# Kernel optimization log

Measured on AMD Instinct MI355X. Metric: run time of the kernel, lower is better.

The kernel has to match this reference:

```python
import jax, jax.numpy as jnp
import numpy as np

THRESH = 0.5
DECAY = 0.2
D_IN = 784
H1 = 2048
H2 = 10
K = 10
U = D_IN + H1
L = 128
B = 1024


def setup_inputs() -> dict:
    key = jax.random.key(0)
    ks = jax.random.split(key, 6)
    inp = jax.random.uniform(ks[0], (B, D_IN), dtype=jnp.float32)
    W1 = jax.random.normal(ks[1], (H1, D_IN), dtype=jnp.float32) * 0.05
    b1 = jnp.zeros((H1,), dtype=jnp.float32)
    W2 = jax.random.normal(ks[2], (H2, H1), dtype=jnp.float32) * 0.05
    b2 = jnp.zeros((H2,), dtype=jnp.float32)
    # core_mem_all[k][u][0] -> sparse-ish per-unit vector, [1] -> count
    core_mem_vec = (jax.random.uniform(ks[3], (K, U, L)) > 0.7).astype(jnp.float32)
    core_mem_cnt = jax.random.randint(ks[4], (K, U), 0, 5).astype(jnp.int32)
    return {"input": inp, "W1": W1, "b1": b1, "W2": W2, "b2": b2,
            "core_mem_vec": core_mem_vec, "core_mem_cnt": core_mem_cnt,
            "time_window": 20}


def act_fun(mem):
    # spike = Heaviside(mem - thresh)
    return (mem > THRESH).astype(mem.dtype)


def reference(input, W1, b1, W2, b2, core_mem_vec, core_mem_cnt, time_window):
    batch, d_in = input.shape
    h1 = W1.shape[0]
    h2 = W2.shape[0]
    Lv = core_mem_vec.shape[-1]

    # Precompute, per (core k, unit u): contribution to count_add_1 / count_add_2
    # when unit u spikes. count_add_1 += (last nonzero index of temp) - 1 when cnt>0;
    # count_add_2 += cnt when cnt>0. Sum over cores up front (loop order irrelevant).
    nz = core_mem_vec != 0                                     # [K,U,L]
    has = nz.any(-1)
    last_idx = Lv - 1 - jnp.argmax(nz[..., ::-1].astype(jnp.int32), axis=-1)  # [K,U]
    active = (core_mem_cnt > 0) & has
    val1 = jnp.where(active, last_idx - 1, 0).sum(0).astype(jnp.float32)      # [U]
    val2 = jnp.where(core_mem_cnt > 0, core_mem_cnt, 0).sum(0).astype(jnp.float32)
    v1x, v1h = val1[:d_in], val1[d_in:]
    v2x, v2h = val2[:d_in], val2[d_in:]

    key = jax.random.key(42)

    def step(carry, t):
        h1m, h1s, h2m, h2s, h2sum, a1, a2, cs = carry
        # Bernoulli rate encoding of the input image
        x = (input > jax.random.uniform(jax.random.fold_in(key, t), input.shape)).astype(jnp.float32)
        # mem_update: mem = mem*decay*(1-spike) + W x + b ; spike = mem > thresh
        h1m = h1m * DECAY * (1.0 - h1s) + x @ W1.T + b1
        h1s = act_fun(h1m)
        h2m = h2m * DECAY * (1.0 - h2s) + h1s @ W2.T + b2
        h2s = act_fun(h2m)
        h2sum = h2sum + h2s
        # vectorized core-memory gather/count: sum per-unit precomputed values
        # over all spiking units, across the batch
        xs = x.sum(0)      # [784] spike counts per input unit this step
        hs = h1s.sum(0)    # [h1]
        a1 = a1 + xs @ v1x + hs @ v1h
        a2 = a2 + xs @ v2x + hs @ v2h
        cs = cs + xs.sum() + hs.sum()
        return (h1m, h1s, h2m, h2s, h2sum, a1, a2, cs), None

    z1 = jnp.zeros((batch, h1), dtype=jnp.float32)
    z2 = jnp.zeros((batch, h2), dtype=jnp.float32)
    carry = (z1, z1, z2, z2, z2, jnp.float32(0), jnp.float32(0), jnp.float32(0))
    carry, _ = jax.lax.scan(step, carry, jnp.arange(time_window))
    _, _, _, _, h2sum, a1, a2, cs = carry
    outputs = h2sum / time_window
    return outputs, a1, a2, cs
```

## Files before the change

kernel.cpp:

```cpp
#include <hip/hip_runtime.h>
#include <cstdint>
#include <cstddef>

static constexpr int D_IN = 784;
static constexpr int H1   = 2048;
static constexpr int H2   = 10;
static constexpr int KK   = 10;
static constexpr int UU   = 2832;
static constexpr int LL   = 128;
static constexpr int BB   = 1024;
static constexpr int TT   = 20;
static constexpr int HALF = BB * D_IN / 2;
static constexpr int KS   = 13;
static constexpr int NLIMB = 3;
static constexpr int NT16 = 128;
static constexpr int MT16 = 64;
static constexpr int PANEL16 = KS * NLIMB * 64;
static constexpr int XA_MT = KS * 64;
static constexpr int NPART_GEN = 2080;
static constexpr int NPART_H1  = 512;
static constexpr int NPART = NPART_GEN + NPART_H1;

static constexpr int BLK_VALS  = UU / 4;
static constexpr int BLK_W2T   = H1 / 256;
static constexpr int BLK_LIMBS = (NT16 * KS) / 4;
static constexpr int BLK_TRANS = 16 * 13;
static constexpr int SETUP_BLOCKS = BLK_VALS + BLK_W2T + BLK_LIMBS + BLK_TRANS;

typedef int v4i  __attribute__((ext_vector_type(4)));

#define MFMA16 __builtin_amdgcn_mfma_i32_16x16x64_i8

__device__ __forceinline__ uint32_t rotl32(uint32_t x, int d) {
  return (x << d) | (x >> (32 - d));
}
__device__ __forceinline__ void threefry2x32(uint32_t k0, uint32_t k1,
                                             uint32_t& x0, uint32_t& x1) {
  uint32_t ks2 = k0 ^ k1 ^ 0x1BD11BDAu;
  x0 += k0; x1 += k1;
#define TF_R(r) { x0 += x1; x1 = rotl32(x1, (r)); x1 ^= x0; }
  TF_R(13) TF_R(15) TF_R(26) TF_R(6)
  x0 += k1;  x1 += ks2 + 1u;
  TF_R(17) TF_R(29) TF_R(16) TF_R(24)
  x0 += ks2; x1 += k0 + 2u;
  TF_R(13) TF_R(15) TF_R(26) TF_R(6)
  x0 += k0;  x1 += k1 + 3u;
  TF_R(17) TF_R(29) TF_R(16) TF_R(24)
  x0 += k1;  x1 += ks2 + 4u;
  TF_R(13) TF_R(15) TF_R(26) TF_R(6)
  x0 += ks2; x1 += k0 + 5u;
#undef TF_R
}
__device__ __forceinline__ float bits_to_unif(uint32_t b) {
  uint32_t fb = (b >> 9) | 0x3F800000u;
  return __uint_as_float(fb) - 1.0f;
}

__device__ __forceinline__ double wave_red(double v) {
  #pragma unroll
  for (int off = 32; off > 0; off >>= 1) v += __shfl_down(v, off, 64);
  return v;
}
__device__ __forceinline__ void block_store3(double s0, double s1, double s2,
                                             double* slot) {
  __shared__ double lds[3][8];
  int lane = threadIdx.x & 63, w = threadIdx.x >> 6;
  int nw = (int)(blockDim.x >> 6);
  s0 = wave_red(s0); s1 = wave_red(s1); s2 = wave_red(s2);
  if (lane == 0) { lds[0][w] = s0; lds[1][w] = s1; lds[2][w] = s2; }
  __syncthreads();
  if (threadIdx.x == 0) {
    double t0 = 0, t1 = 0, t2 = 0;
    for (int i = 0; i < nw; i++) { t0 += lds[0][i]; t1 += lds[1][i]; t2 += lds[2][i]; }
    slot[0] = t0; slot[1] = t1; slot[2] = t2;
  }
}

__global__ __launch_bounds__(256)
void setup(const float* __restrict__ cmv, const int* __restrict__ cmc,
           float* __restrict__ v1, float* __restrict__ v2,
           const float* __restrict__ W2, float* __restrict__ W2T,
           const float* __restrict__ W1, v4i* __restrict__ W1L,
           const float* __restrict__ input, float2* __restrict__ inT2) {
  int bx = blockIdx.x;
  if (bx < BLK_VALS) {
    int u = bx * 4 + (threadIdx.x >> 6);
    int lane = threadIdx.x & 63;
    float acc1 = 0.0f, acc2 = 0.0f;
    for (int k = 0; k < KK; k++) {
      const float* p = cmv + ((size_t)k * UU + u) * LL;
      float a = p[lane];
      float b = p[lane + 64];
      unsigned long long mlo = __ballot(a != 0.0f);
      unsigned long long mhi = __ballot(b != 0.0f);
      int c = cmc[k * UU + u];
      if (c > 0) {
        int last = mhi ? (127 - __builtin_clzll(mhi))
                       : (mlo ? (63 - __builtin_clzll(mlo)) : -1);
        if (last >= 0) acc1 += (float)(last - 1);
        acc2 += (float)c;
      }
    }
    if (lane == 0) { v1[u] = acc1; v2[u] = acc2; }
  } else if (bx < BLK_VALS + BLK_W2T) {
    int i = (bx - BLK_VALS) * 256 + threadIdx.x;
    #pragma unroll
    for (int j = 0; j < H2; j++) W2T[i * H2 + j] = W2[j * H1 + i];
  } else if (bx < BLK_VALS + BLK_W2T + BLK_LIMBS) {
    int tid = (bx - BLK_VALS - BLK_W2T) * 256 + threadIdx.x;
    int lane = tid & 63;
    int tw = tid >> 6;
    int nt = tw / KS, s = tw - nt * KS;
    int n = (nt << 4) + (lane & 15);
    int k0 = (s << 6) + ((lane >> 4) << 4);
    bool valid = (k0 < D_IN);
    union { v4i v; signed char b[16]; } d[NLIMB];
    #pragma unroll
    for (int j = 0; j < 16; j++) {
      long long F = 0;
      if (valid) {
        double w = (double)W1[(size_t)n * D_IN + k0 + j];
        F = llround(w * 0x1p24);
        if (F >  8355711LL) F =  8355711LL;
        if (F < -8421504LL) F = -8421504LL;
      }
      #pragma unroll
      for (int l = 0; l < NLIMB; l++) {
        int dig = (int)((F + 128) & 255) - 128;
        d[l].b[j] = (signed char)dig;
        F = (F - dig) >> 8;
      }
    }
    #pragma unroll
    for (int l = 0; l < NLIMB; l++)
      W1L[(size_t)((nt * KS + s) * NLIMB + l) * 64 + lane] = d[l].v;
  } else {
    int tile = bx - (BLK_VALS + BLK_W2T + BLK_LIMBS);
    int tm = tile / 13, tk = tile % 13;
    int mb = tm * 32, k0 = tk * 64;
    int ncol = (tk == 12) ? 16 : 64;
    __shared__ float ts[64][65];
    int tid = threadIdx.x;
    int nc4 = (tk == 12) ? 4 : 16;
    for (int idx = tid; idx < 64 * nc4; idx += 256) {
      int r = idx / nc4, c4 = idx % nc4;
      int m = mb + (r & 31) + ((r >> 5) << 9);
      const float4* src = (const float4*)(input + (size_t)m * D_IN + k0 + c4 * 4);
      float4 vq = *src;
      ts[r][c4 * 4 + 0] = vq.x; ts[r][c4 * 4 + 1] = vq.y;
      ts[r][c4 * 4 + 2] = vq.z; ts[r][c4 * 4 + 3] = vq.w;
    }
    __syncthreads();
    for (int idx = tid; idx < ncol * 32; idx += 256) {
      int kr = idx >> 5, mc = idx & 31;
      inT2[(size_t)(k0 + kr) * 512 + mb + mc] =
          make_float2(ts[mc][kr], ts[32 + mc][kr]);
    }
  }
}

__global__ __launch_bounds__(256)
void gen_all(const float2* __restrict__ inT2, v4i* __restrict__ XA,
             const float* __restrict__ v1, const float* __restrict__ v2,
             double* __restrict__ gpart) {
  int gw = blockIdx.x * 4 + (threadIdx.x >> 6);
  int lane = threadIdx.x & 63;
  int t = gw / (32 * KS);
  int rem = gw - t * (32 * KS);
  int mt = rem / KS, s = rem - mt * KS;
  int m = (mt << 4) + (lane & 15);
  int k0 = (s << 6) + ((lane >> 4) << 4);
  uint32_t f0 = 0u, f1 = (uint32_t)t;
  threefry2x32(0u, 42u, f0, f1);
  union { v4i v; unsigned char b[16]; } r0, r1;
  double s0 = 0, s1 = 0, s2 = 0;
  if (k0 < D_IN) {
    #pragma unroll
    for (int j = 0; j < 16; j++) {
      int k = k0 + j;
      uint32_t c0 = (uint32_t)(m * D_IN + k), c1 = c0 + (uint32_t)HALF;
      threefry2x32(f0, f1, c0, c1);
      float u0 = bits_to_unif(c0), u1 = bits_to_unif(c1);
      float2 iv = inT2[(size_t)k * 512 + m];
      unsigned char x0 = (iv.x > u0) ? 1 : 0;
      unsigned char x1 = (iv.y > u1) ? 1 : 0;
      r0.b[j] = x0; r1.b[j] = x1;
      double xsum = (double)(x0 + x1);
      s0 += xsum * (double)v1[k];
      s1 += xsum * (double)v2[k];
      s2 += xsum;
    }
  } else {
    r0.v = (v4i){0, 0, 0, 0};
    r1.v = (v4i){0, 0, 0, 0};
  }
  XA[(size_t)((t * MT16 + mt) * KS + s) * 64 + lane] = r0.v;
  XA[(size_t)((t * MT16 + mt + 32) * KS + s) * 64 + lane] = r1.v;
  block_store3(s0, s1, s2, gpart + 3 * (size_t)blockIdx.x);
}

__global__ __launch_bounds__(512, 4)
void h1_all(const v4i* __restrict__ XA, const v4i* __restrict__ W1L,
            const float* __restrict__ b1, uint16_t* __restrict__ bits16,
            const float* __restrict__ v1, const float* __restrict__ v2,
            double* __restrict__ gpart) {
  extern __shared__ v4i bl[];
  int lane = threadIdx.x & 63, wv = threadIdx.x >> 6;
  int id = blockIdx.x + (blockIdx.y << 6);
  int xcd = id & 7;
  int ntb = ((id >> 3) << 1) | (xcd >> 2);
  int mg = xcd & 3;
  int mt0 = (mg << 4) + (wv << 1);
  {
    const v4i* wp = W1L + (size_t)ntb * PANEL16;
    for (int i = threadIdx.x; i < PANEL16; i += 512) bl[i] = wp[i];
  }
  __syncthreads();

  int col = lane & 15;
  int gn = (ntb << 4) + col;
  float bias = b1[gn];
  double v1n = (double)v1[D_IN + gn], v2n = (double)v2[D_IN + gn];
  int scnt = 0;
  float m00 = 0, m01 = 0, m02 = 0, m03 = 0;
  float m10 = 0, m11 = 0, m12 = 0, m13 = 0;
  const v4i* bq = bl + lane;
  int rowg = (lane >> 4) << 2;

  #pragma unroll 1
  for (int t = 0; t < TT; t++) {
    const v4i* a0 = XA + (size_t)((t * MT16 + mt0) * KS) * 64 + lane;
    const v4i* a1 = a0 + KS * 64;
    v4i c00 = {}, c01 = {}, c02 = {};
    v4i c10 = {}, c11 = {}, c12 = {};
    __builtin_amdgcn_s_setprio(1);
    #pragma unroll
    for (int s = 0; s < KS; s++) {
      v4i A0 = a0[s * 64], A1 = a1[s * 64];
      v4i B0 = bq[(s * NLIMB + 0) * 64];
      v4i B1 = bq[(s * NLIMB + 1) * 64];
      v4i B2 = bq[(s * NLIMB + 2) * 64];
      c00 = MFMA16(A0, B0, c00, 0, 0, 0);
      c10 = MFMA16(A1, B0, c10, 0, 0, 0);
      c01 = MFMA16(A0, B1, c01, 0, 0, 0);
      c11 = MFMA16(A1, B1, c11, 0, 0, 0);
      c02 = MFMA16(A0, B2, c02, 0, 0, 0);
      c12 = MFMA16(A1, B2, c12, 0, 0, 0);
    }
    __builtin_amdgcn_s_setprio(0);
    #pragma unroll
    for (int tile = 0; tile < 2; tile++) {
      const v4i& q0 = tile ? c10 : c00;
      const v4i& q1 = tile ? c11 : c01;
      const v4i& q2 = tile ? c12 : c02;
      int gmb = ((mt0 + tile) << 4);
      uint16_t* bp = bits16 + ((size_t)t * BB + gmb) * NT16 + ntb;
      #pragma unroll
      for (int r = 0; r < 4; r++) {
        int val = (int)((uint32_t)q0[r] + ((uint32_t)q1[r] << 8)
                        + ((uint32_t)q2[r] << 16));
        float dot = (float)val * 0x1p-24f + bias;
        float mp = tile ? (r == 0 ? m10 : r == 1 ? m11 : r == 2 ? m12 : m13)
                        : (r == 0 ? m00 : r == 1 ? m01 : r == 2 ? m02 : m03);
        float mnew = (mp > 0.5f) ? dot : fmaf(mp, 0.2f, dot);
        bool sp = (mnew > 0.5f);
        if (tile) { if (r == 0) m10 = mnew; else if (r == 1) m11 = mnew;
                    else if (r == 2) m12 = mnew; else m13 = mnew; }
        else      { if (r == 0) m00 = mnew; else if (r == 1) m01 = mnew;
                    else if (r == 2) m02 = mnew; else m03 = mnew; }
        unsigned long long bm = __ballot(sp);
        if ((lane & 15) == 0)
          bp[(size_t)(rowg + r) * NT16] = (uint16_t)(bm >> lane);
        scnt += sp ? 1 : 0;
      }
    }
  }
  double sc = (double)scnt;
  block_store3(sc * v1n, sc * v2n, sc, gpart + 3 * (size_t)(NPART_GEN + id));
}

__global__ __launch_bounds__(256)
void h2_all(const uint32_t* __restrict__ bits, const float* __restrict__ W2T,
            const float* __restrict__ b2, const double* __restrict__ gpart,
            float* __restrict__ out) {
  int lane = threadIdx.x & 63, wq = threadIdx.x >> 6;
  int b0 = blockIdx.x * 2;
  float w[8][10];
  #pragma unroll
  for (int c = 0; c < 8; c++) {
    int n = (wq << 9) + (c << 6) + lane;
    #pragma unroll
    for (int j = 0; j < 10; j++) w[c][j] = W2T[(size_t)n * H2 + j];
  }
  float m = 0.0f, sp = 0.0f, sm = 0.0f;
  float b2v = (lane < 10) ? b2[lane] : 0.0f;
  __shared__ float part[4][2][10];
  #pragma unroll 1
  for (int t = 0; t < TT; t++) {
    const uint32_t* bt = bits + (size_t)t * (BB * 64);
    #pragma unroll
    for (int r = 0; r < 2; r++) {
      uint32_t myw = bt[(size_t)(b0 + r) * 64 + (wq << 4) + (lane & 15)];
      float p[10];
      #pragma unroll
      for (int j = 0; j < 10; j++) p[j] = 0.0f;
      #pragma unroll
      for (int c = 0; c < 8; c++) {
        uint32_t wd = __shfl(myw, (c << 1) + (lane >> 5), 64);
        float f = (float)((wd >> (lane & 31)) & 1u);
        #pragma unroll
        for (int j = 0; j < 10; j++) p[j] += f * w[c][j];
      }
      #pragma unroll
      for (int j = 0; j < 10; j++) {
        float v = p[j];
        #pragma unroll
        for (int off = 32; off > 0; off >>= 1) v += __shfl_xor(v, off, 64);
        p[j] = v;
      }
      if (lane == 0) {
        #pragma unroll
        for (int j = 0; j < 10; j++) part[wq][r][j] = p[j];
      }
    }
    __syncthreads();
    if (wq < 2 && lane < 10) {
      float red = part[0][wq][lane] + part[1][wq][lane]
                + part[2][wq][lane] + part[3][wq][lane];
      m = m * 0.2f * (1.0f - sp) + red + b2v;
      sp = (m > 0.5f) ? 1.0f : 0.0f;
      sm += sp;
    }
    __syncthreads();
  }
  if (wq < 2 && lane < 10)
    out[(size_t)(b0 + wq) * H2 + lane] = (float)((double)sm / (double)TT);

  if (blockIdx.x == 0) {
    double t0 = 0, t1 = 0, t2 = 0;
    for (int i = threadIdx.x; i < NPART; i += 256) {
      t0 += gpart[3 * (size_t)i];
      t1 += gpart[3 * (size_t)i + 1];
      t2 += gpart[3 * (size_t)i + 2];
    }
    __shared__ double fin[3][4];
    t0 = wave_red(t0); t1 = wave_red(t1); t2 = wave_red(t2);
    if (lane == 0) { fin[0][wq] = t0; fin[1][wq] = t1; fin[2][wq] = t2; }
    __syncthreads();
    if (threadIdx.x == 0) {
      double a = 0, b = 0, cc = 0;
      #pragma unroll
      for (int i = 0; i < 4; i++) { a += fin[0][i]; b += fin[1][i]; cc += fin[2][i]; }
      out[(size_t)BB * H2 + 0] = (float)a;
      out[(size_t)BB * H2 + 1] = (float)b;
      out[(size_t)BB * H2 + 2] = (float)cc;
    }
  }
}

extern "C" void kernel_launch(void* const* d_in, const int* in_sizes, int n_in,
                              void* d_out, int out_size, void* d_ws, size_t ws_size,
                              hipStream_t stream) {
  (void)in_sizes; (void)n_in; (void)out_size; (void)ws_size;
  const float* input = (const float*)d_in[0];
  const float* W1    = (const float*)d_in[1];
  const float* b1    = (const float*)d_in[2];
  const float* W2    = (const float*)d_in[3];
  const float* b2    = (const float*)d_in[4];
  const float* cmv   = (const float*)d_in[5];
  const int*   cmc   = (const int*)d_in[6];

  char* base = (char*)d_ws;
  float*  v1   = (float*)(base + 0);
  float*  v2   = (float*)(base + 11328);
  float*  W2T  = (float*)(base + 22656);
  v4i*    W1L  = (v4i*)(base + 104576);
  v4i*    XA   = (v4i*)(base + 5216384);
  char*   bitsb = base + 22255744;
  double* gpart = (double*)(base + 27498624);
  float2* inT2 = (float2*)bitsb;
  uint16_t* bits16 = (uint16_t*)bitsb;
  uint32_t* bits32 = (uint32_t*)bitsb;

  setup<<<SETUP_BLOCKS, 256, 0, stream>>>(cmv, cmc, v1, v2, W2, W2T, W1, W1L,
                                          input, inT2);
  gen_all<<<NPART_GEN, 256, 0, stream>>>(inT2, XA, v1, v2, gpart);
  h1_all<<<dim3(64, 8), 512, PANEL16 * 16, stream>>>(XA, W1L, b1, bits16, v1, v2,
                                                     gpart);
  h2_all<<<BB / 2, 256, 0, stream>>>(bits32, W2T, b2, gpart, (float*)d_out);
}
```

Baseline: 283.8 us.

## Fuse spike generation into setup kernel and defer input-count reduction to h1

Spike generation is folded into the setup kernel, which removes one kernel launch and the transposed input buffer. Inputs are now read directly as float4 rows. Per-input-unit spike counts are accumulated with ballot/popc and LDS atomics into a per-block count array, and h1_all reduces these counts and applies v1/v2 in its epilogue. This drops the per-block double reductions from the generation stage, but adds extra reads and a sync to h1_all and leaves the input loads uncoalesced along rows.

```diff
diff --git a/kernel.cpp b/kernel.cpp
--- a/kernel.cpp
+++ b/kernel.cpp
@@ -16,16 +16,13 @@
 static constexpr int NT16 = 128;
 static constexpr int MT16 = 64;
 static constexpr int PANEL16 = KS * NLIMB * 64;
-static constexpr int XA_MT = KS * 64;
-static constexpr int NPART_GEN = 2080;
-static constexpr int NPART_H1  = 512;
-static constexpr int NPART = NPART_GEN + NPART_H1;
+static constexpr int NPART = 512;
+static constexpr int NGENB = 2080;
 
 static constexpr int BLK_VALS  = UU / 4;
 static constexpr int BLK_W2T   = H1 / 256;
 static constexpr int BLK_LIMBS = (NT16 * KS) / 4;
-static constexpr int BLK_TRANS = 16 * 13;
-static constexpr int SETUP_BLOCKS = BLK_VALS + BLK_W2T + BLK_LIMBS + BLK_TRANS;
+static constexpr int PREP_BLOCKS = BLK_VALS + BLK_W2T + BLK_LIMBS + NGENB;
 
 typedef int v4i  __attribute__((ext_vector_type(4)));
 
@@ -77,11 +74,12 @@
 }
 
 __global__ __launch_bounds__(256)
-void setup(const float* __restrict__ cmv, const int* __restrict__ cmc,
-           float* __restrict__ v1, float* __restrict__ v2,
-           const float* __restrict__ W2, float* __restrict__ W2T,
-           const float* __restrict__ W1, v4i* __restrict__ W1L,
-           const float* __restrict__ input, float2* __restrict__ inT2) {
+void prep(const float* __restrict__ cmv, const int* __restrict__ cmc,
+          float* __restrict__ v1, float* __restrict__ v2,
+          const float* __restrict__ W2, float* __restrict__ W2T,
+          const float* __restrict__ W1, v4i* __restrict__ W1L,
+          const float* __restrict__ input, v4i* __restrict__ XA,
+          int* __restrict__ xcp) {
   int bx = blockIdx.x;
   if (bx < BLK_VALS) {
     int u = bx * 4 + (threadIdx.x >> 6);
@@ -135,75 +133,62 @@
     for (int l = 0; l < NLIMB; l++)
       W1L[(size_t)((nt * KS + s) * NLIMB + l) * 64 + lane] = d[l].v;
   } else {
-    int tile = bx - (BLK_VALS + BLK_W2T + BLK_LIMBS);
-    int tm = tile / 13, tk = tile % 13;
-    int mb = tm * 32, k0 = tk * 64;
-    int ncol = (tk == 12) ? 16 : 64;
-    __shared__ float ts[64][65];
-    int tid = threadIdx.x;
-    int nc4 = (tk == 12) ? 4 : 16;
-    for (int idx = tid; idx < 64 * nc4; idx += 256) {
-      int r = idx / nc4, c4 = idx % nc4;
-      int m = mb + (r & 31) + ((r >> 5) << 9);
-      const float4* src = (const float4*)(input + (size_t)m * D_IN + k0 + c4 * 4);
-      float4 vq = *src;
-      ts[r][c4 * 4 + 0] = vq.x; ts[r][c4 * 4 + 1] = vq.y;
-      ts[r][c4 * 4 + 2] = vq.z; ts[r][c4 * 4 + 3] = vq.w;
-    }
-    __syncthreads();
-    for (int idx = tid; idx < ncol * 32; idx += 256) {
-      int kr = idx >> 5, mc = idx & 31;
-      inT2[(size_t)(k0 + kr) * 512 + mb + mc] =
-          make_float2(ts[mc][kr], ts[32 + mc][kr]);
-    }
-  }
-}
-
-__global__ __launch_bounds__(256)
-void gen_all(const float2* __restrict__ inT2, v4i* __restrict__ XA,
-             const float* __restrict__ v1, const float* __restrict__ v2,
-             double* __restrict__ gpart) {
-  int gw = blockIdx.x * 4 + (threadIdx.x >> 6);
-  int lane = threadIdx.x & 63;
-  int t = gw / (32 * KS);
-  int rem = gw - t * (32 * KS);
-  int mt = rem / KS, s = rem - mt * KS;
-  int m = (mt << 4) + (lane & 15);
-  int k0 = (s << 6) + ((lane >> 4) << 4);
-  uint32_t f0 = 0u, f1 = (uint32_t)t;
-  threefry2x32(0u, 42u, f0, f1);
-  union { v4i v; unsigned char b[16]; } r0, r1;
-  double s0 = 0, s1 = 0, s2 = 0;
-  if (k0 < D_IN) {
+    int gb = bx - (BLK_VALS + BLK_W2T + BLK_LIMBS);
+    int s = gb % 13, grp = gb / 13;
+    int w = threadIdx.x >> 6, lane = threadIdx.x & 63;
+    int task = grp * 4 + w;
+    int t = task >> 5, mt = task & 31;
+    int m = (mt << 4) + (lane & 15);
+    int g = lane >> 4;
+    int k0 = (s << 6) + (g << 4);
+    bool valid = (k0 < D_IN);
+    __shared__ int xc[64];
+    if (threadIdx.x < 64) xc[threadIdx.x] = 0;
+    __syncthreads();
+    uint32_t f0 = 0u, f1 = (uint32_t)t;
+    threefry2x32(0u, 42u, f0, f1);
+    const float4* P0 = (const float4*)(input + (valid ? (size_t)m * D_IN + k0 : 0));
+    const float4* P1 = (const float4*)(input + (valid ? (size_t)(m + 512) * D_IN + k0 : 0));
+    float i0v[16], i1v[16];
+    #pragma unroll
+    for (int q = 0; q < 4; q++) {
+      float4 a4 = P0[q], b4 = P1[q];
+      i0v[q * 4 + 0] = a4.x; i0v[q * 4 + 1] = a4.y;
+      i0v[q * 4 + 2] = a4.z; i0v[q * 4 + 3] = a4.w;
+      i1v[q * 4 + 0] = b4.x; i1v[q * 4 + 1] = b4.y;
+      i1v[q * 4 + 2] = b4.z; i1v[q * 4 + 3] = b4.w;
+    }
+    union { v4i v; unsigned char b[16]; } r0, r1;
     #pragma unroll
     for (int j = 0; j < 16; j++) {
       int k = k0 + j;
       uint32_t c0 = (uint32_t)(m * D_IN + k), c1 = c0 + (uint32_t)HALF;
       threefry2x32(f0, f1, c0, c1);
       float u0 = bits_to_unif(c0), u1 = bits_to_unif(c1);
-      float2 iv = inT2[(size_t)k * 512 + m];
-      unsigned char x0 = (iv.x > u0) ? 1 : 0;
-      unsigned char x1 = (iv.y > u1) ? 1 : 0;
-      r0.b[j] = x0; r1.b[j] = x1;
-      double xsum = (double)(x0 + x1);
-      s0 += xsum * (double)v1[k];
-      s1 += xsum * (double)v2[k];
-      s2 += xsum;
-    }
-  } else {
-    r0.v = (v4i){0, 0, 0, 0};
-    r1.v = (v4i){0, 0, 0, 0};
-  }
-  XA[(size_t)((t * MT16 + mt) * KS + s) * 64 + lane] = r0.v;
-  XA[(size_t)((t * MT16 + mt + 32) * KS + s) * 64 + lane] = r1.v;
-  block_store3(s0, s1, s2, gpart + 3 * (size_t)blockIdx.x);
+      bool x0 = valid && (i0v[j] > u0);
+      bool x1 = valid && (i1v[j] > u1);
+      r0.b[j] = x0 ? 1 : 0;
+      r1.b[j] = x1 ? 1 : 0;
+      unsigned long long bm0 = __ballot(x0);
+      unsigned long long bm1 = __ballot(x1);
+      if ((lane & 15) == 0) {
+        int cnt = __popc((uint32_t)((bm0 >> (g * 16)) & 0xFFFFu))
+                + __popc((uint32_t)((bm1 >> (g * 16)) & 0xFFFFu));
+        if (cnt) atomicAdd(&xc[(g << 4) + j], cnt);
+      }
+    }
+    XA[(size_t)((t * MT16 + mt) * KS + s) * 64 + lane] = r0.v;
+    XA[(size_t)((t * MT16 + mt + 32) * KS + s) * 64 + lane] = r1.v;
+    __syncthreads();
+    if (threadIdx.x < 64) xcp[(size_t)gb * 64 + threadIdx.x] = xc[threadIdx.x];
+  }
 }
 
 __global__ __launch_bounds__(512, 4)
 void h1_all(const v4i* __restrict__ XA, const v4i* __restrict__ W1L,
             const float* __restrict__ b1, uint16_t* __restrict__ bits16,
             const float* __restrict__ v1, const float* __restrict__ v2,
-            double* __restrict__ gpart) {
+            const int* __restrict__ xcp, double* __restrict__ gpart) {
   extern __shared__ v4i bl[];
   int lane = threadIdx.x & 63, wv = threadIdx.x >> 6;
   int id = blockIdx.x + (blockIdx.y << 6);
@@ -275,8 +260,33 @@
       }
     }
   }
+
+  double e0 = 0, e1 = 0, e2 = 0;
+  {
+    int half = threadIdx.x >> 8;
+    int gi = threadIdx.x & 255;
+    int k = 2 * id + half;
+    int xcv = 0;
+    if (id < 416 && gi < 160) {
+      int s = k >> 6, q = k & 63;
+      xcv = xcp[((size_t)(gi * 13 + s) << 6) + q];
+    }
+    #pragma unroll
+    for (int off = 32; off > 0; off >>= 1) xcv += __shfl_down(xcv, off, 64);
+    __shared__ int xcs[8];
+    if (lane == 0) xcs[wv] = xcv;
+    __syncthreads();
+    if (threadIdx.x == 0 && id < 416) {
+      int xc0 = xcs[0] + xcs[1] + xcs[2] + xcs[3];
+      int xc1 = xcs[4] + xcs[5] + xcs[6] + xcs[7];
+      int kk0 = 2 * id, kk1 = 2 * id + 1;
+      e0 = (double)xc0 * (double)v1[kk0] + (double)xc1 * (double)v1[kk1];
+      e1 = (double)xc0 * (double)v2[kk0] + (double)xc1 * (double)v2[kk1];
+      e2 = (double)(xc0 + xc1);
+    }
+  }
   double sc = (double)scnt;
-  block_store3(sc * v1n, sc * v2n, sc, gpart + 3 * (size_t)(NPART_GEN + id));
+  block_store3(sc * v1n + e0, sc * v2n + e1, sc + e2, gpart + 3 * (size_t)id);
 }
 
 __global__ __launch_bounds__(256)
@@ -376,16 +386,14 @@
   float*  W2T  = (float*)(base + 22656);
   v4i*    W1L  = (v4i*)(base + 104576);
   v4i*    XA   = (v4i*)(base + 5216384);
-  char*   bitsb = base + 22255744;
-  double* gpart = (double*)(base + 27498624);
-  float2* inT2 = (float2*)bitsb;
-  uint16_t* bits16 = (uint16_t*)bitsb;
-  uint32_t* bits32 = (uint32_t*)bitsb;
-
-  setup<<<SETUP_BLOCKS, 256, 0, stream>>>(cmv, cmc, v1, v2, W2, W2T, W1, W1L,
-                                          input, inT2);
-  gen_all<<<NPART_GEN, 256, 0, stream>>>(inT2, XA, v1, v2, gpart);
+  uint16_t* bits16 = (uint16_t*)(base + 22255744);
+  int*    xcp  = (int*)(base + 27498624);
+  double* gpart = (double*)(base + 28031104);
+  const uint32_t* bits32 = (const uint32_t*)(base + 22255744);
+
+  prep<<<PREP_BLOCKS, 256, 0, stream>>>(cmv, cmc, v1, v2, W2, W2T, W1, W1L,
+                                        input, XA, xcp);
   h1_all<<<dim3(64, 8), 512, PANEL16 * 16, stream>>>(XA, W1L, b1, bits16, v1, v2,
-                                                     gpart);
+                                                     xcp, gpart);
   h2_all<<<BB / 2, 256, 0, stream>>>(bits32, W2T, b2, gpart, (float*)d_out);
 }
```

New measurement: 277.7 us. 2.1% less time.
